# Optimization experiments

Measured on AMD Instinct MI355X. Metric: run time of the kernel, lower is better.

The kernel has to match this reference:

```python
import jax, jax.numpy as jnp
import numpy as np

N, D, H, O, E = 50000, 128, 256, 128, 800000


def setup_inputs() -> dict:
    key = jax.random.key(0)
    ks = jax.random.split(key, 8)
    x = jax.random.normal(ks[0], (N, D), dtype=jnp.float32)
    edge_index = jax.random.randint(ks[1], (2, E), 0, N, dtype=jnp.int64)
    s = lambda k, shp: jax.random.normal(k, shp, dtype=jnp.float32) / np.sqrt(shp[0])
    return {
        "x": x,
        "edge_index": edge_index,
        "W1_l": s(ks[2], (D, H)),
        "W1_r": s(ks[3], (D, H)),
        "b1": jnp.zeros((H,), jnp.float32),
        "W2_l": s(ks[4], (H, O)),
        "W2_r": s(ks[5], (H, O)),
        "b2": jnp.zeros((O,), jnp.float32),
    }


def _sage_conv(x, src, dst, W_l, W_r, b, n_nodes):
    # mean aggregation of source messages into destination nodes
    agg = jax.ops.segment_sum(x[src], dst, num_segments=n_nodes)  # [N, F]
    cnt = jax.ops.segment_sum(jnp.ones(src.shape[0], x.dtype), dst,
                              num_segments=n_nodes)               # [N]
    agg = agg / jnp.maximum(cnt, 1.0)[:, None]
    # lin_l(agg) + lin_r(x); lin_l carries the bias (PyG SAGEConv default)
    return agg @ W_l + b + x @ W_r


def reference(x, edge_index, W1_l, W1_r, b1, W2_l, W2_r, b2):
    src, dst = edge_index[0], edge_index[1]
    h = jax.nn.relu(_sage_conv(x, src, dst, W1_l, W1_r, b1, N))
    out = _sage_conv(h, src, dst, W2_l, W2_r, b2, N)
    return out
```

## Files before the change

kernel.cpp:

```cpp
#include <hip/hip_runtime.h>


#define CAP 64
#define NB 98
#define BSH 9
#define BCAP 9216
#define CHUNK 2048

typedef __attribute__((ext_vector_type(8))) short short8;
typedef __attribute__((ext_vector_type(8))) unsigned short ushort8;
typedef __attribute__((ext_vector_type(4))) float f32x4;

__device__ __forceinline__ unsigned short f2bf(float f) {
  unsigned u = __builtin_bit_cast(unsigned, f);
  u += 0x7fff + ((u >> 16) & 1);
  return (unsigned short)(u >> 16);
}
__device__ __forceinline__ float bf2f(unsigned v) {
  return __builtin_bit_cast(float, v << 16);
}

__device__ __forceinline__ void gload_lds16(const unsigned short* g, char* l) {
  __builtin_amdgcn_global_load_lds(
      (const __attribute__((address_space(1))) unsigned int*)g,
      (__attribute__((address_space(3))) unsigned int*)l, 16, 0, 0);
}

__global__ __launch_bounds__(256) void prep_kernel(
    const float* __restrict__ x, unsigned short* __restrict__ xb,
    const float* __restrict__ W1l, const float* __restrict__ W1r,
    const float* __restrict__ W2l, const float* __restrict__ W2r,
    unsigned short* __restrict__ Wt1, unsigned short* __restrict__ Wt2,
    int* __restrict__ bcursor, unsigned short* __restrict__ hw, int n8, int N) {
  const int b = blockIdx.x;
  const int t = threadIdx.x;
  if (b == 0) {
    if (t < 128) bcursor[t] = 0;
    if (t < 64) {
      reinterpret_cast<unsigned*>(xb + (size_t)N * 128)[t] = 0u;
      reinterpret_cast<unsigned*>(hw + (size_t)N * 128)[t] = 0u;
    }
  }
  if (b < 256) {
    int idx = b * 256 + t;
    int ch = idx >> 8, k = idx & 255;
    Wt1[idx] = f2bf((k < 128) ? W1l[k * 256 + ch] : W1r[(k - 128) * 256 + ch]);
    Wt2[idx] = f2bf((ch < 128) ? W2l[k * 128 + ch] : W2r[k * 128 + (ch - 128)]);
  } else {
    int i = (b - 256) * 256 + t;
    if (i < n8) {
      const float4* p = reinterpret_cast<const float4*>(x) + (size_t)i * 2;
      float4 a = p[0], bb = p[1];
      union { unsigned short u[8]; int4 v; } r;
      r.u[0]=f2bf(a.x); r.u[1]=f2bf(a.y); r.u[2]=f2bf(a.z); r.u[3]=f2bf(a.w);
      r.u[4]=f2bf(bb.x); r.u[5]=f2bf(bb.y); r.u[6]=f2bf(bb.z); r.u[7]=f2bf(bb.w);
      reinterpret_cast<int4*>(xb)[i] = r.v;
    }
  }
}

__global__ __launch_bounds__(256) void bucket_kernel(
    const int* __restrict__ src, const int* __restrict__ dst,
    int* __restrict__ bcursor, unsigned* __restrict__ buckets, int E) {
  __shared__ unsigned pack[CHUNK];
  __shared__ unsigned char binarr[CHUNK];
  __shared__ unsigned sorted[CHUNK];
  __shared__ unsigned char sbin[CHUNK];
  __shared__ int hist[NB];
  __shared__ int scn[NB + 1];
  __shared__ int gbase[NB];
  const int t = threadIdx.x;
  const int e0 = blockIdx.x * CHUNK;
  const int n = min(CHUNK, E - e0);

  for (int i = t; i < NB; i += 256) hist[i] = 0;
  __syncthreads();
  for (int i = t; i < n; i += 256) {
    int s = src[e0 + i];
    int d = dst[e0 + i];
    int b = d >> BSH;
    pack[i] = ((unsigned)(d & 511) << 16) | (unsigned)s;
    binarr[i] = (unsigned char)b;
    atomicAdd(&hist[b], 1);
  }
  __syncthreads();
  if (t == 0) {
    int a = 0;
    for (int b = 0; b < NB; ++b) { scn[b] = a; a += hist[b]; }
    scn[NB] = a;
  }
  __syncthreads();
  if (t < NB) { gbase[t] = atomicAdd(&bcursor[t], hist[t]); hist[t] = 0; }
  __syncthreads();
  for (int i = t; i < n; i += 256) {
    int b = binarr[i];
    int pos = scn[b] + atomicAdd(&hist[b], 1);
    sorted[pos] = pack[i];
    sbin[pos] = (unsigned char)b;
  }
  __syncthreads();
  for (int i = t; i < n; i += 256) {
    int b = sbin[i];
    int off = gbase[b] + (i - scn[b]);
    if (off < BCAP) buckets[(size_t)b * BCAP + off] = sorted[i];
  }
}

__global__ __launch_bounds__(256) void csr_kernel(
    const int* __restrict__ bcursor, const unsigned* __restrict__ buckets,
    unsigned short* __restrict__ elist, int* __restrict__ deg, int N) {
  __shared__ unsigned short csr[128 * CAP];
  __shared__ int cur[128];
  const int t = threadIdx.x;
  const int b = blockIdx.x >> 2;
  const int q = blockIdx.x & 3;
  if (t < 128) cur[t] = 0;
  __syncthreads();
  const int cnt = min(bcursor[b], BCAP);
  const unsigned* bp = buckets + (size_t)b * BCAP;
  for (int i = t; i < cnt; i += 256) {
    unsigned p = bp[i];
    int lo = p >> 16;
    if ((lo >> 7) == q) {
      int r = lo & 127;
      int pos = atomicAdd(&cur[r], 1);
      if (pos < CAP) csr[r * CAP + pos] = (unsigned short)(p & 0xffffu);
    }
  }
  __syncthreads();
  if (t < 128) {
    int d = min(cur[t], CAP);
    int dgc = (d + 7) & ~7;
    if (dgc < 8) dgc = 8;
    if (dgc > CAP) dgc = CAP;
    for (int p = d; p < dgc; ++p) csr[t * CAP + p] = (unsigned short)N;
  }
  __syncthreads();
  const int node0 = (b << BSH) + (q << 7);
  const int nn = min(128, N - node0);
  if (nn <= 0) return;
  if (t < nn) deg[node0 + t] = min(cur[t], CAP);
  int4* dst4 = reinterpret_cast<int4*>(elist + (size_t)node0 * CAP);
  const int4* src4 = reinterpret_cast<const int4*>(csr);
  for (int i = t; i < nn * 8; i += 256) dst4[i] = src4[i];
}

#define GLD(P, EV) \
  P##0 = f[(size_t)(EV)[0] * 64 + lane]; P##1 = f[(size_t)(EV)[1] * 64 + lane]; \
  P##2 = f[(size_t)(EV)[2] * 64 + lane]; P##3 = f[(size_t)(EV)[3] * 64 + lane]; \
  P##4 = f[(size_t)(EV)[4] * 64 + lane]; P##5 = f[(size_t)(EV)[5] * 64 + lane]; \
  P##6 = f[(size_t)(EV)[6] * 64 + lane]; P##7 = f[(size_t)(EV)[7] * 64 + lane];
#define ACC(P) \
  s0x += bf2f(P##0 & 0xffffu); s0y += bf2f(P##0 >> 16); \
  s1x += bf2f(P##1 & 0xffffu); s1y += bf2f(P##1 >> 16); \
  s2x += bf2f(P##2 & 0xffffu); s2y += bf2f(P##2 >> 16); \
  s3x += bf2f(P##3 & 0xffffu); s3y += bf2f(P##3 >> 16); \
  s0x += bf2f(P##4 & 0xffffu); s0y += bf2f(P##4 >> 16); \
  s1x += bf2f(P##5 & 0xffffu); s1y += bf2f(P##5 >> 16); \
  s2x += bf2f(P##6 & 0xffffu); s2y += bf2f(P##6 >> 16); \
  s3x += bf2f(P##7 & 0xffffu); s3y += bf2f(P##7 >> 16);

template<int MODE>
__global__ __launch_bounds__(256) void aggregate_kernel(
    const unsigned short* __restrict__ feat, const int* __restrict__ deg_,
    const unsigned short* __restrict__ elist, const unsigned short* __restrict__ hr,
    const float* __restrict__ bias, void* __restrict__ outp, int N) {
  const int node = (blockIdx.x * blockDim.x + threadIdx.x) >> 6;
  const int lane = threadIdx.x & 63;
  if (node >= N) return;
  const int deg = deg_[node];
  int dgc = (deg + 7) & ~7; if (dgc < 8) dgc = 8;
  const unsigned* f = reinterpret_cast<const unsigned*>(feat);
  const int4* el4 = reinterpret_cast<const int4*>(elist + (size_t)node * CAP);
  int4 p0 = el4[0], p1 = el4[1], p2 = el4[2], p3 = el4[3],
       p4 = el4[4], p5 = el4[5], p6 = el4[6], p7 = el4[7];
  ushort8 c0 = __builtin_bit_cast(ushort8, p0), c1 = __builtin_bit_cast(ushort8, p1),
          c2 = __builtin_bit_cast(ushort8, p2), c3 = __builtin_bit_cast(ushort8, p3),
          c4 = __builtin_bit_cast(ushort8, p4), c5 = __builtin_bit_cast(ushort8, p5),
          c6 = __builtin_bit_cast(ushort8, p6), c7 = __builtin_bit_cast(ushort8, p7);
  float s0x=0.f,s0y=0.f,s1x=0.f,s1y=0.f,s2x=0.f,s2y=0.f,s3x=0.f,s3y=0.f;
  unsigned a0,a1,a2,a3,a4,a5,a6,a7, b0,b1,b2,b3,b4,b5,b6,b7;
  GLD(a, c0);
  if (dgc > 8)  { GLD(b, c1); }
  ACC(a);
  if (dgc > 16) { GLD(a, c2); }
  if (dgc > 8)  { ACC(b); }
  if (dgc > 24) { GLD(b, c3); }
  if (dgc > 16) { ACC(a); }
  if (dgc > 32) { GLD(a, c4); }
  if (dgc > 24) { ACC(b); }
  if (dgc > 40) { GLD(b, c5); }
  if (dgc > 32) { ACC(a); }
  if (dgc > 48) { GLD(a, c6); }
  if (dgc > 40) { ACC(b); }
  if (dgc > 56) { GLD(b, c7); }
  if (dgc > 48) { ACC(a); }
  if (dgc > 56) { ACC(b); }
  float inv = 1.0f / (float)max(deg, 1);
  float rx = (s0x + s1x + s2x + s3x) * inv;
  float ry = (s0y + s1y + s2y + s3y) * inv;
  if constexpr (MODE == 0) {
    unsigned r = (unsigned)f2bf(rx) | ((unsigned)f2bf(ry) << 16);
    reinterpret_cast<unsigned*>(outp)[(size_t)node * 64 + lane] = r;
  } else {
    unsigned res = reinterpret_cast<const unsigned*>(hr)[(size_t)node * 64 + lane];
    float2 bb = reinterpret_cast<const float2*>(bias)[lane];
    float2 o;
    o.x = rx + bf2f(res & 0xffffu) + bb.x;
    o.y = ry + bf2f(res >> 16) + bb.y;
    reinterpret_cast<float2*>(outp)[(size_t)node * 64 + lane] = o;
  }
}

__global__ __launch_bounds__(256, 2) void fused_gemm_kernel(
    const unsigned short* __restrict__ aggb, const unsigned short* __restrict__ xb,
    const unsigned short* __restrict__ Wt1, const unsigned short* __restrict__ Wt2,
    const float* __restrict__ b1,
    unsigned short* __restrict__ hw, unsigned short* __restrict__ hr, int N) {
  __shared__ int4 As4[512];
  __shared__ int4 Bs4[2048];
  __shared__ int4 hL4[2048];
  char* As = reinterpret_cast<char*>(As4);
  char* Bs = reinterpret_cast<char*>(Bs4);
  char* hL = reinterpret_cast<char*>(hL4);
  const int t = threadIdx.x;
  const int lane = t & 63;
  const int hi = lane >> 4;
  const int lo = lane & 15;
  const int wv = t >> 6;
  const int n0 = blockIdx.x * 64;
  const int cw = wv * 64;
  const int rb = lane >> 3;
  const int swz = ((lane & 7) ^ rb) * 8;

  f32x4 acc[4][4];
  #pragma unroll
  for (int m = 0; m < 4; ++m)
    #pragma unroll
    for (int n = 0; n < 4; ++n)
      acc[m][n] = (f32x4){0.f, 0.f, 0.f, 0.f};

  for (int k0 = 0; k0 < 256; k0 += 64) {
    const unsigned short* Asrc = (k0 < 128) ? aggb : xb;
    const int kk0 = k0 & 127;
    #pragma unroll
    for (int si = 0; si < 2; ++si) {
      int s = wv * 2 + si;
      int r = s * 8 + rb;
      int row = n0 + r; if (row >= N) row = N - 1;
      gload_lds16(Asrc + (size_t)row * 128 + kk0 + swz, As + s * 1024);
    }
    #pragma unroll
    for (int si = 0; si < 8; ++si) {
      int s = wv * 8 + si;
      int cc = s * 8 + rb;
      gload_lds16(Wt1 + (size_t)cc * 256 + k0 + swz, Bs + s * 1024);
    }
    __syncthreads();
    #pragma unroll
    for (int kk = 0; kk < 64; kk += 32) {
      const int kb = (kk + hi * 8) * 2;
      short8 af[4], bfr[4];
      #pragma unroll
      for (int m = 0; m < 4; ++m) {
        int r = m * 16 + lo;
        af[m] = *reinterpret_cast<const short8*>(As + r * 128 + (kb ^ ((r & 7) << 4)));
      }
      #pragma unroll
      for (int n = 0; n < 4; ++n) {
        int c = cw + n * 16 + lo;
        bfr[n] = *reinterpret_cast<const short8*>(Bs + c * 128 + (kb ^ ((c & 7) << 4)));
      }
      #pragma unroll
      for (int m = 0; m < 4; ++m)
        #pragma unroll
        for (int n = 0; n < 4; ++n)
          acc[m][n] = __builtin_amdgcn_mfma_f32_16x16x32_bf16(af[m], bfr[n], acc[m][n], 0, 0, 0);
    }
    __syncthreads();
  }

  #pragma unroll
  for (int n = 0; n < 4; ++n) {
    const int col = cw + n * 16 + lo;
    const float bv = b1[col];
    const int seg = col >> 6;
    const int wb = (col & 63) * 2;
    #pragma unroll
    for (int m = 0; m < 4; ++m) {
      f32x4 v = acc[m][n];
      #pragma unroll
      for (int j = 0; j < 4; ++j) {
        int row = m * 16 + hi * 4 + j;
        float f = fmaxf(v[j] + bv, 0.0f);
        *reinterpret_cast<unsigned short*>(
            hL + row * 512 + seg * 128 + (wb ^ ((row & 7) << 4))) = f2bf(f);
      }
    }
  }
  __syncthreads();

  f32x4 acc2[4][4];
  #pragma unroll
  for (int m = 0; m < 4; ++m)
    #pragma unroll
    for (int n = 0; n < 4; ++n)
      acc2[m][n] = (f32x4){0.f, 0.f, 0.f, 0.f};

  for (int k0 = 0; k0 < 256; k0 += 64) {
    #pragma unroll
    for (int si = 0; si < 8; ++si) {
      int s = wv * 8 + si;
      int cc = s * 8 + rb;
      gload_lds16(Wt2 + (size_t)cc * 256 + k0 + swz, Bs + s * 1024);
    }
    __syncthreads();
    #pragma unroll
    for (int kk = 0; kk < 64; kk += 32) {
      const int kb = (kk + hi * 8) * 2;
      short8 af[4], bfr[4];
      #pragma unroll
      for (int m = 0; m < 4; ++m) {
        int r = m * 16 + lo;
        af[m] = *reinterpret_cast<const short8*>(hL + r * 512 + k0 * 2 + (kb ^ ((r & 7) << 4)));
      }
      #pragma unroll
      for (int n = 0; n < 4; ++n) {
        int c = cw + n * 16 + lo;
        bfr[n] = *reinterpret_cast<const short8*>(Bs + c * 128 + (kb ^ ((c & 7) << 4)));
      }
      #pragma unroll
      for (int m = 0; m < 4; ++m)
        #pragma unroll
        for (int n = 0; n < 4; ++n)
          acc2[m][n] = __builtin_amdgcn_mfma_f32_16x16x32_bf16(af[m], bfr[n], acc2[m][n], 0, 0, 0);
    }
    __syncthreads();
  }

  unsigned short* dstp = (cw < 128) ? hw : hr;
  const int cbase = cw & 127;
  #pragma unroll
  for (int n = 0; n < 4; ++n) {
    const int col = cbase + n * 16 + lo;
    #pragma unroll
    for (int m = 0; m < 4; ++m) {
      f32x4 v = acc2[m][n];
      #pragma unroll
      for (int j = 0; j < 4; ++j) {
        int row = n0 + m * 16 + hi * 4 + j;
        if (row < N) dstp[(size_t)row * 128 + col] = f2bf(v[j]);
      }
    }
  }
}

extern "C" void kernel_launch(void* const* d_in, const int* in_sizes, int n_in,
                              void* d_out, int out_size, void* d_ws, size_t ws_size,
                              hipStream_t stream) {
  const float* x   = (const float*)d_in[0];
  const int*   ei  = (const int*)d_in[1];
  const float* W1l = (const float*)d_in[2];
  const float* W1r = (const float*)d_in[3];
  const float* b1  = (const float*)d_in[4];
  const float* W2l = (const float*)d_in[5];
  const float* W2r = (const float*)d_in[6];
  const float* b2  = (const float*)d_in[7];
  float* out = (float*)d_out;

  const int N = in_sizes[0] / 128;
  const int E = in_sizes[1] / 2;
  const int* src = ei;
  const int* dst = ei + E;

  int* iws = (int*)d_ws;
  int* bcursor = iws;
  unsigned* buckets = (unsigned*)(iws + 128);
  int* deg = (int*)(buckets + (size_t)NB * BCAP);
  unsigned short* elist = (unsigned short*)(deg + ((N + 64) & ~63));
  unsigned short* xb   = elist + (size_t)N * CAP;
  unsigned short* aggb = xb + (size_t)(N + 8) * 128;
  unsigned short* hw   = aggb + (size_t)N * 128;
  unsigned short* hr   = hw + (size_t)(N + 8) * 128;
  unsigned short* Wt1  = hr + (size_t)N * 128;
  unsigned short* Wt2  = Wt1 + 65536;

  const int n8 = N * 128 / 8;
  prep_kernel<<<256 + (n8 + 255) / 256, 256, 0, stream>>>(
      x, xb, W1l, W1r, W2l, W2r, Wt1, Wt2, bcursor, hw, n8, N);

  bucket_kernel<<<(E + CHUNK - 1) / CHUNK, 256, 0, stream>>>(src, dst, bcursor, buckets, E);
  csr_kernel<<<NB * 4, 256, 0, stream>>>(bcursor, buckets, elist, deg, N);

  const int aggBlocks = (N * 64 + 255) / 256;
  const int MB = (N + 63) / 64;

  aggregate_kernel<0><<<aggBlocks, 256, 0, stream>>>(xb, deg, elist, nullptr, nullptr, (void*)aggb, N);
  fused_gemm_kernel<<<MB, 256, 0, stream>>>(aggb, xb, Wt1, Wt2, b1, hw, hr, N);
  aggregate_kernel<1><<<aggBlocks, 256, 0, stream>>>(hw, deg, elist, hr, b2, (void*)out, N);
}
```

Before: 126.1 us.

## Merge bucketing into prep kernel with per-chunk slots, drop global cursor atomics

Folds the edge-bucketing pass into the prep kernel so one launch does bucketing, weight transpose and bf16 conversion of x. Each edge chunk now writes to fixed per-(bucket, chunk) slots of capacity 64 with a per-chunk count, which removes the global cursor atomics and the separate cursor-zeroing dependency. The CSR kernel then scans every chunk's slot region and skips unused entries. In exchange it reads a larger sparse bucket area, and a bucket/chunk pair with more than 64 edges would silently drop edges (about 21 are expected on average).

```diff
diff --git a/kernel.cpp b/kernel.cpp
--- a/kernel.cpp
+++ b/kernel.cpp
@@ -4,7 +4,7 @@
 #define CAP 64
 #define NB 98
 #define BSH 9
-#define BCAP 9216
+#define SCAP 64
 #define CHUNK 2048
 
 typedef __attribute__((ext_vector_type(8))) short short8;
@@ -26,28 +26,69 @@
       (__attribute__((address_space(3))) unsigned int*)l, 16, 0, 0);
 }
 
-__global__ __launch_bounds__(256) void prep_kernel(
+__global__ __launch_bounds__(256) void build_kernel(
+    const int* __restrict__ src, const int* __restrict__ dst,
+    unsigned* __restrict__ buckets2, unsigned short* __restrict__ cnt16, int nblk,
     const float* __restrict__ x, unsigned short* __restrict__ xb,
     const float* __restrict__ W1l, const float* __restrict__ W1r,
     const float* __restrict__ W2l, const float* __restrict__ W2r,
     unsigned short* __restrict__ Wt1, unsigned short* __restrict__ Wt2,
-    int* __restrict__ bcursor, unsigned short* __restrict__ hw, int n8, int N) {
+    unsigned short* __restrict__ hw, int E, int n8, int N) {
+  __shared__ unsigned pack[CHUNK];
+  __shared__ unsigned char binarr[CHUNK];
+  __shared__ unsigned sorted[CHUNK];
+  __shared__ unsigned char sbin[CHUNK];
+  __shared__ int hist[NB];
+  __shared__ int scn[NB + 1];
   const int b = blockIdx.x;
   const int t = threadIdx.x;
-  if (b == 0) {
-    if (t < 128) bcursor[t] = 0;
-    if (t < 64) {
-      reinterpret_cast<unsigned*>(xb + (size_t)N * 128)[t] = 0u;
-      reinterpret_cast<unsigned*>(hw + (size_t)N * 128)[t] = 0u;
-    }
-  }
-  if (b < 256) {
-    int idx = b * 256 + t;
+
+  if (b < nblk) {
+    const int e0 = b * CHUNK;
+    const int n = min(CHUNK, E - e0);
+    for (int i = t; i < NB; i += 256) hist[i] = 0;
+    __syncthreads();
+    for (int i = t; i < n; i += 256) {
+      int s = src[e0 + i];
+      int d = dst[e0 + i];
+      int bb = d >> BSH;
+      pack[i] = ((unsigned)(d & 511) << 16) | (unsigned)s;
+      binarr[i] = (unsigned char)bb;
+      atomicAdd(&hist[bb], 1);
+    }
+    __syncthreads();
+    if (t == 0) {
+      int a = 0;
+      for (int bb = 0; bb < NB; ++bb) { scn[bb] = a; a += hist[bb]; }
+      scn[NB] = a;
+    }
+    __syncthreads();
+    if (t < NB) hist[t] = 0;
+    __syncthreads();
+    for (int i = t; i < n; i += 256) {
+      int bb = binarr[i];
+      int pos = scn[bb] + atomicAdd(&hist[bb], 1);
+      sorted[pos] = pack[i];
+      sbin[pos] = (unsigned char)bb;
+    }
+    __syncthreads();
+    for (int i = t; i < n; i += 256) {
+      int bb = sbin[i];
+      int off = i - scn[bb];
+      if (off < SCAP) buckets2[((size_t)bb * nblk + b) * SCAP + off] = sorted[i];
+    }
+    if (t < NB) cnt16[t * nblk + b] = (unsigned short)min(scn[t + 1] - scn[t], SCAP);
+  } else if (b < nblk + 256) {
+    int idx = (b - nblk) * 256 + t;
     int ch = idx >> 8, k = idx & 255;
     Wt1[idx] = f2bf((k < 128) ? W1l[k * 256 + ch] : W1r[(k - 128) * 256 + ch]);
     Wt2[idx] = f2bf((ch < 128) ? W2l[k * 128 + ch] : W2r[k * 128 + (ch - 128)]);
   } else {
-    int i = (b - 256) * 256 + t;
+    if (b == nblk + 256 && t < 64) {
+      reinterpret_cast<unsigned*>(xb + (size_t)N * 128)[t] = 0u;
+      reinterpret_cast<unsigned*>(hw + (size_t)N * 128)[t] = 0u;
+    }
+    int i = (b - nblk - 256) * 256 + t;
     if (i < n8) {
       const float4* p = reinterpret_cast<const float4*>(x) + (size_t)i * 2;
       float4 a = p[0], bb = p[1];
@@ -59,72 +100,31 @@
   }
 }
 
-__global__ __launch_bounds__(256) void bucket_kernel(
-    const int* __restrict__ src, const int* __restrict__ dst,
-    int* __restrict__ bcursor, unsigned* __restrict__ buckets, int E) {
-  __shared__ unsigned pack[CHUNK];
-  __shared__ unsigned char binarr[CHUNK];
-  __shared__ unsigned sorted[CHUNK];
-  __shared__ unsigned char sbin[CHUNK];
-  __shared__ int hist[NB];
-  __shared__ int scn[NB + 1];
-  __shared__ int gbase[NB];
-  const int t = threadIdx.x;
-  const int e0 = blockIdx.x * CHUNK;
-  const int n = min(CHUNK, E - e0);
-
-  for (int i = t; i < NB; i += 256) hist[i] = 0;
-  __syncthreads();
-  for (int i = t; i < n; i += 256) {
-    int s = src[e0 + i];
-    int d = dst[e0 + i];
-    int b = d >> BSH;
-    pack[i] = ((unsigned)(d & 511) << 16) | (unsigned)s;
-    binarr[i] = (unsigned char)b;
-    atomicAdd(&hist[b], 1);
-  }
-  __syncthreads();
-  if (t == 0) {
-    int a = 0;
-    for (int b = 0; b < NB; ++b) { scn[b] = a; a += hist[b]; }
-    scn[NB] = a;
-  }
-  __syncthreads();
-  if (t < NB) { gbase[t] = atomicAdd(&bcursor[t], hist[t]); hist[t] = 0; }
-  __syncthreads();
-  for (int i = t; i < n; i += 256) {
-    int b = binarr[i];
-    int pos = scn[b] + atomicAdd(&hist[b], 1);
-    sorted[pos] = pack[i];
-    sbin[pos] = (unsigned char)b;
-  }
-  __syncthreads();
-  for (int i = t; i < n; i += 256) {
-    int b = sbin[i];
-    int off = gbase[b] + (i - scn[b]);
-    if (off < BCAP) buckets[(size_t)b * BCAP + off] = sorted[i];
-  }
-}
-
 __global__ __launch_bounds__(256) void csr_kernel(
-    const int* __restrict__ bcursor, const unsigned* __restrict__ buckets,
-    unsigned short* __restrict__ elist, int* __restrict__ deg, int N) {
+    const unsigned short* __restrict__ cnt16, const unsigned* __restrict__ buckets2,
+    unsigned short* __restrict__ elist, int* __restrict__ deg, int N, int nblk) {
   __shared__ unsigned short csr[128 * CAP];
   __shared__ int cur[128];
+  __shared__ unsigned short cnts[512];
   const int t = threadIdx.x;
   const int b = blockIdx.x >> 2;
   const int q = blockIdx.x & 3;
   if (t < 128) cur[t] = 0;
+  for (int i = t; i < nblk; i += 256) cnts[i] = cnt16[b * nblk + i];
   __syncthreads();
-  const int cnt = min(bcursor[b], BCAP);
-  const unsigned* bp = buckets + (size_t)b * BCAP;
-  for (int i = t; i < cnt; i += 256) {
-    unsigned p = bp[i];
-    int lo = p >> 16;
-    if ((lo >> 7) == q) {
-      int r = lo & 127;
-      int pos = atomicAdd(&cur[r], 1);
-      if (pos < CAP) csr[r * CAP + pos] = (unsigned short)(p & 0xffffu);
+  const int tot = nblk * SCAP;
+  const unsigned* bp = buckets2 + (size_t)b * nblk * SCAP;
+  for (int idx = t; idx < tot; idx += 256) {
+    int blk = idx >> 6;
+    int slot = idx & (SCAP - 1);
+    if (slot < (int)cnts[blk]) {
+      unsigned p = bp[idx];
+      int lo = p >> 16;
+      if ((lo >> 7) == q) {
+        int r = lo & 127;
+        int pos = atomicAdd(&cur[r], 1);
+        if (pos < CAP) csr[r * CAP + pos] = (unsigned short)(p & 0xffffu);
+      }
     }
   }
   __syncthreads();
@@ -372,11 +372,12 @@
   const int E = in_sizes[1] / 2;
   const int* src = ei;
   const int* dst = ei + E;
+  const int nblk = (E + CHUNK - 1) / CHUNK;
 
   int* iws = (int*)d_ws;
-  int* bcursor = iws;
-  unsigned* buckets = (unsigned*)(iws + 128);
-  int* deg = (int*)(buckets + (size_t)NB * BCAP);
+  unsigned short* cnt16 = (unsigned short*)iws;
+  unsigned* buckets2 = (unsigned*)(cnt16 + (((size_t)NB * nblk + 63) & ~(size_t)63));
+  int* deg = (int*)(buckets2 + (size_t)NB * nblk * SCAP);
   unsigned short* elist = (unsigned short*)(deg + ((N + 64) & ~63));
   unsigned short* xb   = elist + (size_t)N * CAP;
   unsigned short* aggb = xb + (size_t)(N + 8) * 128;
@@ -386,11 +387,11 @@
   unsigned short* Wt2  = Wt1 + 65536;
 
   const int n8 = N * 128 / 8;
-  prep_kernel<<<256 + (n8 + 255) / 256, 256, 0, stream>>>(
-      x, xb, W1l, W1r, W2l, W2r, Wt1, Wt2, bcursor, hw, n8, N);
-
-  bucket_kernel<<<(E + CHUNK - 1) / CHUNK, 256, 0, stream>>>(src, dst, bcursor, buckets, E);
-  csr_kernel<<<NB * 4, 256, 0, stream>>>(bcursor, buckets, elist, deg, N);
+  const int buildBlocks = nblk + 256 + (n8 + 255) / 256;
+  build_kernel<<<buildBlocks, 256, 0, stream>>>(
+      src, dst, buckets2, cnt16, nblk, x, xb, W1l, W1r, W2l, W2r, Wt1, Wt2, hw,
+      E, n8, N);
+  csr_kernel<<<NB * 4, 256, 0, stream>>>(cnt16, buckets2, elist, deg, N, nblk);
 
   const int aggBlocks = (N * 64 + 255) / 256;
   const int MB = (N + 63) / 64;
```

Result: slower. 142.9 us (+13.4%).
